# Kernel tuning notes

Hardware: AMD Instinct MI355X
Metric: run time of the kernel (lower is better)

The kernel has to match this reference:

```python
import jax, jax.numpy as jnp
import numpy as np
from jax import lax

M = 4  # signature truncation level (matches init kwarg m)


def setup_inputs() -> dict:
    key = jax.random.key(0)
    x = jax.random.normal(key, (2048, 256, 10), dtype=jnp.float32)
    return {"x": x}


def _signature(x, m):
    """Truncated path signature via Chen's identity.

    x: (B, L, d) path. Returns (B, sum_{k=1..m} d^k), levels 1..m concatenated
    in row-major tensor order (matching iisignature.sig layout).
    Recurrence: S <- S \otimes exp(dx_t), where exp(v) has level-k term v^{\otimes k}/k!.
    """
    B, L, d = x.shape
    dx = x[:, 1:, :] - x[:, :-1, :]  # (B, L-1, d) path increments

    def step(carry, v):
        # carry: tuple of (B, d^k) signature levels; v: (B, d) increment
        # segment signature: seg[k] = v^{\otimes(k+1)} / (k+1)!
        seg = [v]
        for k in range(1, m):
            seg.append((seg[-1][:, :, None] * v[:, None, :]).reshape(B, -1) / (k + 1))
        # truncated tensor-algebra product: new_k = S_k + seg_k + sum_i S_i (x) seg_{k-1-i}
        new = []
        for k in range(m):
            t = carry[k] + seg[k]
            for i in range(k):
                t = t + (carry[i][:, :, None] * seg[k - 1 - i][:, None, :]).reshape(B, -1)
            new.append(t)
        return tuple(new), None

    init = tuple(jnp.zeros((B, d ** (k + 1)), x.dtype) for k in range(m))
    final, _ = lax.scan(step, init, jnp.moveaxis(dx, 1, 0))
    return jnp.concatenate(final, axis=-1)


def reference(x):
    return _signature(x, M)
```

## Files before the change

kernel.cpp:

```cpp
#include <hip/hip_runtime.h>


#define SIG 11110

typedef short bf16x8 __attribute__((ext_vector_type(8)));
typedef float f32x4  __attribute__((ext_vector_type(4)));

__device__ __forceinline__ unsigned cvt_pk2(float lo, float hi) {
    unsigned r;
    asm("v_cvt_pk_bf16_f32 %0, %1, %2" : "=v"(r) : "v"(lo), "v"(hi));
    return r;
}
__device__ __forceinline__ unsigned split_pack(float a) {
    const float hi = __uint_as_float(__float_as_uint(a) & 0xFFFF0000u);
    return cvt_pk2(hi, a - hi);
}

template<int MI, int NI>
__device__ __forceinline__ void consume(const unsigned* __restrict__ Pb,
                                        const unsigned* __restrict__ Qb,
                                        int r0, int c0, int lane,
                                        f32x4 (&acc)[MI][NI]) {
    const int slot = lane >> 4, rr = lane & 15;
    bf16x8 Bf[NI];
    #pragma unroll
    for (int ni = 0; ni < NI; ++ni)
        Bf[ni] = *(const bf16x8*)(Qb + slot * 448 + (c0 + ni * 16 + rr) * 4);
    #pragma unroll
    for (int mi = 0; mi < MI; ++mi) {
        const bf16x8 Af = *(const bf16x8*)(Pb + slot * 448 + (r0 + mi * 16 + rr) * 4);
        #pragma unroll
        for (int ni = 0; ni < NI; ++ni)
            acc[mi][ni] = __builtin_amdgcn_mfma_f32_16x16x32_bf16(Af, Bf[ni], acc[mi][ni], 0, 0, 0);
    }
}

template<int MI, int NI>
__device__ __forceinline__ void write_seg(int r0, int c0, int lane,
                                          const f32x4 (&acc)[MI][NI],
                                          float* __restrict__ out, size_t base) {
    #pragma unroll
    for (int mi = 0; mi < MI; ++mi) {
        #pragma unroll
        for (int ni = 0; ni < NI; ++ni) {
            #pragma unroll
            for (int r = 0; r < 4; ++r) {
                const int m = r0 + mi * 16 + (lane >> 4) * 4 + r;
                const int n = c0 + ni * 16 + (lane & 15);
                if (m < 100) {
                    if (n < 100)      out[base + 1110 + m * 100 + n]         = acc[mi][ni][r];
                    else if (n < 110) out[base + 110  + m * 10  + (n - 100)] = acc[mi][ni][r];
                }
            }
        }
    }
}

__device__ __forceinline__ void produce(int ch, const float* __restrict__ vt,
                                        unsigned* __restrict__ Pb,
                                        unsigned* __restrict__ Qb,
                                        bool isPair, bool isQ,
                                        int prow, int qrow, int i1, int i2,
                                        float& s1f, float& Rv, float& Ds) {
    if (isPair) {
        const float4 a0 = *(const float4*)(vt + i1 * 260 + ch * 8);
        const float4 a1 = *(const float4*)(vt + i1 * 260 + ch * 8 + 4);
        const float4 b0 = *(const float4*)(vt + i2 * 260 + ch * 8);
        const float4 b1 = *(const float4*)(vt + i2 * 260 + ch * 8 + 4);
        const float v1[8] = {a0.x,a0.y,a0.z,a0.w,a1.x,a1.y,a1.z,a1.w};
        const float v2[8] = {b0.x,b0.y,b0.z,b0.w,b1.x,b1.y,b1.z,b1.w};
        unsigned q0 = 0, q1 = 0;
        #pragma unroll
        for (int tl = 0; tl < 8; ++tl) {
            const float vi = v1[tl], vj = v2[tl];
            const float r1 = vi * vj;
            const float r2 = s1f * vj;
            const float a  = fmaf(r1, 1.f/6.f, fmaf(r2, 0.5f, Ds));
            const unsigned pa = split_pack(a), pr = cvt_pk2(r1, r2);
            Ds += fmaf(0.5f, r1, r2);
            s1f += vi;
            if ((tl & 1) == 0) { q0 = pa; q1 = pr; }
            else *(uint4*)&Pb[(tl >> 1) * 448 + prow * 4] = make_uint4(q0, q1, pa, pr);
        }
    } else if (isQ) {
        const float4 a0 = *(const float4*)(vt + i1 * 260 + ch * 8);
        const float4 a1 = *(const float4*)(vt + i1 * 260 + ch * 8 + 4);
        const float4 b0 = *(const float4*)(vt + i2 * 260 + ch * 8);
        const float4 b1 = *(const float4*)(vt + i2 * 260 + ch * 8 + 4);
        const float v1[8] = {a0.x,a0.y,a0.z,a0.w,a1.x,a1.y,a1.z,a1.w};
        const float v2[8] = {b0.x,b0.y,b0.z,b0.w,b1.x,b1.y,b1.z,b1.w};
        unsigned q0 = 0, q1 = 0;
        #pragma unroll
        for (int tl = 0; tl < 8; ++tl) {
            const float vk = v1[tl], vl = v2[tl];
            const float w  = vk * vl;
            const float m2 = fmaf(-0.5f, vl, Rv);
            Rv -= vl;
            const float uw = vk * m2;
            const unsigned pu = cvt_pk2(uw, uw);
            const unsigned pw = cvt_pk2(w * (-1.f/24.f), w * (-1.f/12.f));
            if ((tl & 1) == 0) { q0 = pu; q1 = pw; }
            else *(uint4*)&Qb[(tl >> 1) * 448 + qrow * 4] = make_uint4(q0, q1, pu, pw);
        }
    }
}

template<int MIA, int NIA, int R0A, int C0A, int MIB, int NIB, int R0B, int C0B>
__device__ __forceinline__ void run_wave(const float* __restrict__ vt,
                                         unsigned (&Pl)[2][1792],
                                         unsigned (&Ql)[2][1792],
                                         bool isPair, bool isQ,
                                         int prow, int qrow, int i1, int i2,
                                         float s1f, float Rv,
                                         int lane, float* __restrict__ out, size_t base) {
    float Ds = 0.f;
    f32x4 accA[MIA][NIA];
    #pragma unroll
    for (int mi = 0; mi < MIA; ++mi)
        #pragma unroll
        for (int ni = 0; ni < NIA; ++ni) accA[mi][ni] = (f32x4){0.f, 0.f, 0.f, 0.f};
    constexpr int MB = (MIB > 0) ? MIB : 1;
    constexpr int NB = (NIB > 0) ? NIB : 1;
    f32x4 accB[MB][NB];
    if constexpr (MIB > 0) {
        #pragma unroll
        for (int mi = 0; mi < MB; ++mi)
            #pragma unroll
            for (int ni = 0; ni < NB; ++ni) accB[mi][ni] = (f32x4){0.f, 0.f, 0.f, 0.f};
    }

    produce(0, vt, Pl[0], Ql[0], isPair, isQ, prow, qrow, i1, i2, s1f, Rv, Ds);
    __syncthreads();

    for (int ch = 0; ch < 32; ++ch) {
        const unsigned* Pb = Pl[ch & 1];
        const unsigned* Qb = Ql[ch & 1];
        consume<MIA, NIA>(Pb, Qb, R0A, C0A, lane, accA);
        if constexpr (MIB > 0) consume<MIB, NIB>(Pb, Qb, R0B, C0B, lane, accB);
        if (ch < 31)
            produce(ch + 1, vt, Pl[(ch + 1) & 1], Ql[(ch + 1) & 1],
                    isPair, isQ, prow, qrow, i1, i2, s1f, Rv, Ds);
        __syncthreads();
    }

    if (isPair) out[base + 10 + prow] = Ds;
    write_seg<MIA, NIA>(R0A, C0A, lane, accA, out, base);
    if constexpr (MIB > 0) write_seg<MIB, NIB>(R0B, C0B, lane, accB, out, base);
}

__global__ __launch_bounds__(256, 4)
void sig_mfma16(const float* __restrict__ xg, float* __restrict__ out) {
    __shared__ float    vt[11 * 260];
    __shared__ unsigned Pl[2][1792];
    __shared__ unsigned Ql[2][1792];

    const int tid  = threadIdx.x;
    const int b    = blockIdx.x;
    const int lane = tid & 63;
    const int wv   = tid >> 6;
    const float* __restrict__ xb = xg + (size_t)b * 2560;

    for (int e = tid; e < 2550; e += 256) {
        const int t = e / 10, d = e - t * 10;
        vt[d * 260 + t] = xb[e + 10] - xb[e];
    }
    if (tid < 10) vt[tid * 260 + 255] = 0.f;
    for (int e = tid; e < 260; e += 256) vt[10 * 260 + e] = 0.f;
    for (int e = tid; e < 384; e += 256) {
        const int buf = e / 192, r = e % 192, slot = r / 48, rem = r % 48;
        Pl[buf][slot * 448 + (100 + rem / 4) * 4 + (rem & 3)] = 0u;
    }
    if (tid < 64) {
        const int buf = tid / 32, r = tid % 32, slot = r / 8, rem = r % 8;
        Ql[buf][slot * 448 + (110 + rem / 4) * 4 + (rem & 3)] = 0u;
    }
    __syncthreads();

    const int  pid    = tid - 128;
    const bool isPair = (pid >= 0) && (pid < 100);
    const bool isQ    = (tid < 110);
    const int  prow   = isPair ? pid : 0;
    const int  qrow   = tid;

    int i1 = 0, i2 = 0;
    if (isPair)          { i1 = pid / 10; i2 = pid - i1 * 10; }
    else if (tid < 100)  { i1 = tid / 10; i2 = tid - i1 * 10; }
    else if (tid < 110)  { i1 = tid - 100; i2 = 10; }

    const float s1f = 0.f;
    float Rv = 0.f;
    if (tid < 100)      Rv = xb[2550 + i2] - xb[i2];
    else if (tid < 110) Rv = 1.f;
    const size_t base = (size_t)b * SIG;

    if      (wv == 0) run_wave<4, 3,  0, 48, 0, 0,  0,  0>(vt, Pl, Ql, isPair, isQ,
                          prow, qrow, i1, i2, s1f, Rv, lane, out, base);
    else if (wv == 1) run_wave<3, 3, 64, 48, 4, 1,  0, 96>(vt, Pl, Ql, isPair, isQ,
                          prow, qrow, i1, i2, s1f, Rv, lane, out, base);
    else if (wv == 2) run_wave<4, 3,  0,  0, 0, 0,  0,  0>(vt, Pl, Ql, isPair, isQ,
                          prow, qrow, i1, i2, s1f, Rv, lane, out, base);
    else              run_wave<3, 3, 64,  0, 3, 1, 64, 96>(vt, Pl, Ql, isPair, isQ,
                          prow, qrow, i1, i2, s1f, Rv, lane, out, base);

    if (tid < 10) out[base + tid] = xb[2550 + tid] - xb[tid];
}

extern "C" void kernel_launch(void* const* d_in, const int* in_sizes, int n_in,
                              void* d_out, int out_size, void* d_ws, size_t ws_size,
                              hipStream_t stream) {
    const float* x = (const float*)d_in[0];
    float* out = (float*)d_out;
    const int B = in_sizes[0] / 2560;
    sig_mfma16<<<B, 256, 0, stream>>>(x, out);
}
```

Baseline: 82.87 us.

## Pack 10 timesteps per MFMA K-chunk using 3-wide operand encoding

Measured after the change: 76.34 us. 7.9% less time.

```diff
diff --git a/kernel.cpp b/kernel.cpp
--- a/kernel.cpp
+++ b/kernel.cpp
@@ -2,6 +2,7 @@
 
 
 #define SIG 11110
+#define NCH 26
 
 typedef short bf16x8 __attribute__((ext_vector_type(8)));
 typedef float f32x4  __attribute__((ext_vector_type(4)));
@@ -10,10 +11,6 @@
     unsigned r;
     asm("v_cvt_pk_bf16_f32 %0, %1, %2" : "=v"(r) : "v"(lo), "v"(hi));
     return r;
-}
-__device__ __forceinline__ unsigned split_pack(float a) {
-    const float hi = __uint_as_float(__float_as_uint(a) & 0xFFFF0000u);
-    return cvt_pk2(hi, a - hi);
 }
 
 template<int MI, int NI>
@@ -62,46 +59,65 @@
                                         bool isPair, bool isQ,
                                         int prow, int qrow, int i1, int i2,
                                         float& s1f, float& Rv, float& Ds) {
+    float v1[10], v2[10];
+    {
+        const float* p1 = vt + i1 * 260 + ch * 10;
+        const float* p2 = vt + i2 * 260 + ch * 10;
+        #pragma unroll
+        for (int k = 0; k < 5; ++k) {
+            const float2 x = *(const float2*)(p1 + 2 * k);
+            const float2 y = *(const float2*)(p2 + 2 * k);
+            v1[2 * k] = x.x; v1[2 * k + 1] = x.y;
+            v2[2 * k] = y.x; v2[2 * k + 1] = y.y;
+        }
+    }
     if (isPair) {
-        const float4 a0 = *(const float4*)(vt + i1 * 260 + ch * 8);
-        const float4 a1 = *(const float4*)(vt + i1 * 260 + ch * 8 + 4);
-        const float4 b0 = *(const float4*)(vt + i2 * 260 + ch * 8);
-        const float4 b1 = *(const float4*)(vt + i2 * 260 + ch * 8 + 4);
-        const float v1[8] = {a0.x,a0.y,a0.z,a0.w,a1.x,a1.y,a1.z,a1.w};
-        const float v2[8] = {b0.x,b0.y,b0.z,b0.w,b1.x,b1.y,b1.z,b1.w};
-        unsigned q0 = 0, q1 = 0;
-        #pragma unroll
-        for (int tl = 0; tl < 8; ++tl) {
+        float ah[10], al[10], rr[10];
+        #pragma unroll
+        for (int tl = 0; tl < 10; ++tl) {
             const float vi = v1[tl], vj = v2[tl];
             const float r1 = vi * vj;
             const float r2 = s1f * vj;
             const float a  = fmaf(r1, 1.f/6.f, fmaf(r2, 0.5f, Ds));
-            const unsigned pa = split_pack(a), pr = cvt_pk2(r1, r2);
+            const float hi = __uint_as_float(__float_as_uint(a) & 0xFFFF0000u);
+            ah[tl] = hi; al[tl] = a - hi;
+            rr[tl] = fmaf(2.f, r2, r1);
             Ds += fmaf(0.5f, r1, r2);
             s1f += vi;
-            if ((tl & 1) == 0) { q0 = pa; q1 = pr; }
-            else *(uint4*)&Pb[(tl >> 1) * 448 + prow * 4] = make_uint4(q0, q1, pa, pr);
-        }
+        }
+        unsigned wd[15];
+        #pragma unroll
+        for (int m = 0; m < 5; ++m) {
+            wd[3 * m + 0] = cvt_pk2(ah[2 * m],     al[2 * m]);
+            wd[3 * m + 1] = cvt_pk2(rr[2 * m],     ah[2 * m + 1]);
+            wd[3 * m + 2] = cvt_pk2(al[2 * m + 1], rr[2 * m + 1]);
+        }
+        *(uint4*)&Pb[0 * 448 + prow * 4] = make_uint4(wd[0],  wd[1],  wd[2],  wd[3]);
+        *(uint4*)&Pb[1 * 448 + prow * 4] = make_uint4(wd[4],  wd[5],  wd[6],  wd[7]);
+        *(uint4*)&Pb[2 * 448 + prow * 4] = make_uint4(wd[8],  wd[9],  wd[10], wd[11]);
+        *(uint4*)&Pb[3 * 448 + prow * 4] = make_uint4(wd[12], wd[13], wd[14], 0u);
     } else if (isQ) {
-        const float4 a0 = *(const float4*)(vt + i1 * 260 + ch * 8);
-        const float4 a1 = *(const float4*)(vt + i1 * 260 + ch * 8 + 4);
-        const float4 b0 = *(const float4*)(vt + i2 * 260 + ch * 8);
-        const float4 b1 = *(const float4*)(vt + i2 * 260 + ch * 8 + 4);
-        const float v1[8] = {a0.x,a0.y,a0.z,a0.w,a1.x,a1.y,a1.z,a1.w};
-        const float v2[8] = {b0.x,b0.y,b0.z,b0.w,b1.x,b1.y,b1.z,b1.w};
-        unsigned q0 = 0, q1 = 0;
-        #pragma unroll
-        for (int tl = 0; tl < 8; ++tl) {
+        float uw[10], mw[10];
+        #pragma unroll
+        for (int tl = 0; tl < 10; ++tl) {
             const float vk = v1[tl], vl = v2[tl];
             const float w  = vk * vl;
             const float m2 = fmaf(-0.5f, vl, Rv);
             Rv -= vl;
-            const float uw = vk * m2;
-            const unsigned pu = cvt_pk2(uw, uw);
-            const unsigned pw = cvt_pk2(w * (-1.f/24.f), w * (-1.f/12.f));
-            if ((tl & 1) == 0) { q0 = pu; q1 = pw; }
-            else *(uint4*)&Qb[(tl >> 1) * 448 + qrow * 4] = make_uint4(q0, q1, pu, pw);
-        }
+            uw[tl] = vk * m2;
+            mw[tl] = w * (-1.f/24.f);
+        }
+        unsigned wd[15];
+        #pragma unroll
+        for (int m = 0; m < 5; ++m) {
+            wd[3 * m + 0] = cvt_pk2(uw[2 * m],     uw[2 * m]);
+            wd[3 * m + 1] = cvt_pk2(mw[2 * m],     uw[2 * m + 1]);
+            wd[3 * m + 2] = cvt_pk2(uw[2 * m + 1], mw[2 * m + 1]);
+        }
+        *(uint4*)&Qb[0 * 448 + qrow * 4] = make_uint4(wd[0],  wd[1],  wd[2],  wd[3]);
+        *(uint4*)&Qb[1 * 448 + qrow * 4] = make_uint4(wd[4],  wd[5],  wd[6],  wd[7]);
+        *(uint4*)&Qb[2 * 448 + qrow * 4] = make_uint4(wd[8],  wd[9],  wd[10], wd[11]);
+        *(uint4*)&Qb[3 * 448 + qrow * 4] = make_uint4(wd[12], wd[13], wd[14], 0u);
     }
 }
 
@@ -132,12 +148,12 @@
     produce(0, vt, Pl[0], Ql[0], isPair, isQ, prow, qrow, i1, i2, s1f, Rv, Ds);
     __syncthreads();
 
-    for (int ch = 0; ch < 32; ++ch) {
+    for (int ch = 0; ch < NCH; ++ch) {
         const unsigned* Pb = Pl[ch & 1];
         const unsigned* Qb = Ql[ch & 1];
         consume<MIA, NIA>(Pb, Qb, R0A, C0A, lane, accA);
         if constexpr (MIB > 0) consume<MIB, NIB>(Pb, Qb, R0B, C0B, lane, accB);
-        if (ch < 31)
+        if (ch < NCH - 1)
             produce(ch + 1, vt, Pl[(ch + 1) & 1], Ql[(ch + 1) & 1],
                     isPair, isQ, prow, qrow, i1, i2, s1f, Rv, Ds);
         __syncthreads();
@@ -149,7 +165,7 @@
 }
 
 __global__ __launch_bounds__(256, 4)
-void sig_mfma16(const float* __restrict__ xg, float* __restrict__ out) {
+void sig_mfma17(const float* __restrict__ xg, float* __restrict__ out) {
     __shared__ float    vt[11 * 260];
     __shared__ unsigned Pl[2][1792];
     __shared__ unsigned Ql[2][1792];
@@ -164,7 +180,7 @@
         const int t = e / 10, d = e - t * 10;
         vt[d * 260 + t] = xb[e + 10] - xb[e];
     }
-    if (tid < 10) vt[tid * 260 + 255] = 0.f;
+    if (tid < 55) vt[(tid / 5) * 260 + 255 + (tid % 5)] = 0.f;
     for (int e = tid; e < 260; e += 256) vt[10 * 260 + e] = 0.f;
     for (int e = tid; e < 384; e += 256) {
         const int buf = e / 192, r = e % 192, slot = r / 48, rem = r % 48;
@@ -211,5 +227,5 @@
     const float* x = (const float*)d_in[0];
     float* out = (float*)d_out;
     const int B = in_sizes[0] / 2560;
-    sig_mfma16<<<B, 256, 0, stream>>>(x, out);
-}
+    sig_mfma17<<<B, 256, 0, stream>>>(x, out);
+}
```
